# Kernel tuning notes

Hardware: AMD Instinct MI355X
Metric: run time of the kernel (lower is better)

## Reference

```python
import jax, jax.numpy as jnp
import numpy as np

START = 5.0
STEP = 8
SIZE = 256
STOP = SIZE // 2 - 1.0  # self.stop = int(size/2) - 1.0
# Original loops over tf.linspace(s, stop, step) and truncates each value to int.
US = [int(v) for v in np.linspace(START, STOP, STEP)]


def _block_mask(w, h, u):
    # Boolean block of ones of size (2u+1)^2 centered at (w//2, h//2).
    # Original: dd[half_w-u:half_w+u+1, half_h-u:half_h+u+1] = 1, then keeps
    # only that region of the shifted spectrum (ideal low-pass filter).
    m = np.zeros((w, h), dtype=np.float32)
    m[w // 2 - u: w // 2 + u + 1, h // 2 - u: h // 2 + u + 1] = 1.0
    return jnp.asarray(m)


def setup_inputs() -> dict:
    key = jax.random.key(0)
    x = jax.random.normal(key, (64, SIZE, SIZE, 1), dtype=jnp.float32)
    return {"x": x}


def reference(x):
    n, w, h, c = x.shape  # c == 1
    im = x[..., 0].astype(jnp.complex64)  # [n, w, h]
    # FFT is identical across loop iterations in the original; hoist it.
    # fftshift/ifftshift over all axes in TF cancel on the batch axis, so
    # shifting only the spatial axes is mathematically identical.
    freq = jnp.fft.fftshift(jnp.fft.fft2(im), axes=(-2, -1))
    outs = [x]
    for u in US:  # small fixed loop over STEP cutoff radii
        mask = _block_mask(w, h, u)
        low = freq * mask.astype(jnp.complex64)  # keep low frequencies only
        out = jnp.real(jnp.fft.ifft2(jnp.fft.ifftshift(low, axes=(-2, -1))))
        outs.append(out.astype(x.dtype)[..., None])
    return jnp.concatenate(outs, axis=-1)  # [n, w, h, STEP+1]
```

## Files before the change

### kernel.cpp

```cpp
#include <hip/hip_runtime.h>

typedef __attribute__((ext_vector_type(4))) float          f32x4;
typedef __attribute__((ext_vector_type(2))) float          f32x2;
typedef __attribute__((ext_vector_type(4))) unsigned int   u32x4;
typedef __attribute__((ext_vector_type(4))) unsigned short u16x4;
typedef __attribute__((ext_vector_type(2))) unsigned short u16x2;

typedef const unsigned int __attribute__((address_space(1)))* gas_ptr;
typedef unsigned int __attribute__((address_space(3)))*       las_ptr;

#define PI_F 3.14159265358979f

__device__ __forceinline__ unsigned short f2bf(float f) {
    unsigned int x = __float_as_uint(f);
    unsigned int r = ((x >> 16) & 1u) + 0x7fffu;
    return (unsigned short)((x + r) >> 16);
}
__device__ __forceinline__ float bf2f(unsigned short v) {
    return __uint_as_float((unsigned int)v << 16);
}
__device__ __forceinline__ void mfma16(f32x4& c, u32x4 a, u32x4 b) {
    asm volatile("v_mfma_f32_16x16x32_bf16 %0, %1, %2, %0"
                 : "+v"(c) : "v"(a), "v"(b));
}
__device__ __forceinline__ void gload16(const void* g, void* l) {
    __builtin_amdgcn_global_load_lds((gas_ptr)g, (las_ptr)l, 16, 0, 0);
}

#define SWZ(r, cb) (((unsigned)(r) * 128u) + ((unsigned)(cb) ^ ((((unsigned)(r)) & 7u) << 4)))

__global__ void prep(const float* __restrict__ x, unsigned short* __restrict__ H,
                     unsigned short* __restrict__ Xb, float* __restrict__ out,
                     int write_c0) {
    int b = blockIdx.x;
    if (b < 2048) {
        const int US[8] = {5, 22, 39, 57, 74, 92, 109, 127};
        int idx = b * 256 + threadIdx.x;
        int u = idx >> 16;
        int i = (idx >> 8) & 255, js = idx & 255;
        int jl = js ^ ((i & 7) << 3);
        int d = (i - jl) & 255;
        int m = 2 * US[u] + 1;
        float h;
        if (d == 0) {
            h = (float)m * (1.0f / 256.0f);
        } else {
            int t = (m * d) & 511;
            float num = sinf((float)t * (PI_F / 256.0f));
            float den = sinf((float)d * (PI_F / 256.0f));
            h = num / (256.0f * den);
        }
        H[idx] = f2bf(h);
    } else {
        int idx = (b - 2048) * 256 + threadIdx.x;
        f32x4 v = ((const f32x4*)x)[idx];
        u16x4 o = { f2bf(v.x), f2bf(v.y), f2bf(v.z), f2bf(v.w) };
        int n = idx >> 14;
        int t = idx & 16383;
        int i = t >> 6;
        int jlin = (t & 63) * 4;
        int js = jlin ^ ((i & 7) << 3);
        *(u16x4*)(Xb + (size_t)n * 65536 + i * 256 + js) = o;
        if (write_c0) {
            size_t g = (size_t)idx * 4;
            out[(g + 0) * 9] = v.x;
            out[(g + 1) * 9] = v.y;
            out[(g + 2) * 9] = v.z;
            out[(g + 3) * 9] = v.w;
        }
    }
}

__global__ void __launch_bounds__(512) stage12(const unsigned short* __restrict__ Xb,
                                               const unsigned short* __restrict__ H,
                                               unsigned short* __restrict__ Zb,
                                               float* __restrict__ fOut,
                                               int mode, int u_fixed) {
    extern __shared__ char smem[];
    char* sStage = smem;
    char* sHalf  = smem + 32768;
    char* sT     = smem + 49152;

    int n, u, jh;
    if (u_fixed >= 0) {
        n = blockIdx.x >> 1; jh = blockIdx.x & 1; u = u_fixed;
    } else {
        int swz = (blockIdx.x & 7) * 128 + (blockIdx.x >> 3);
        n = swz >> 4; u = (swz >> 1) & 7; jh = swz & 1;
    }

    const char* Xn = (const char*)(Xb + (size_t)n * 65536);
    const char* Hu = (const char*)(H + (size_t)u * 65536);

    const int tid  = threadIdx.x;
    const int lane = tid & 63;
    const int w    = tid >> 6;
    const int lrow = lane & 15;
    const int lk   = lane >> 4;
    const int srow = lane >> 3, sch = lane & 7;

    f32x4 acc[4][4];
#pragma unroll
    for (int a = 0; a < 4; ++a)
#pragma unroll
        for (int b = 0; b < 4; ++b) acc[a][b] = (f32x4){0.f, 0.f, 0.f, 0.f};

    const int wiA = w >> 1, wjA = w & 1;
    for (int kt = 0; kt < 4; ++kt) {
        if (kt) __syncthreads();
#pragma unroll
        for (int q = 0; q < 4; ++q) {
            int r = (w * 4 + q) * 8 + srow;
            gload16(Xn + r * 512 + kt * 128 + sch * 16, sStage + (w * 4 + q) * 1024);
        }
#pragma unroll
        for (int q = 0; q < 2; ++q) {
            int r = jh * 128 + (w * 2 + q) * 8 + srow;
            gload16(Hu + r * 512 + kt * 128 + sch * 16, sHalf + (w * 2 + q) * 1024);
        }
        __syncthreads();
#pragma unroll
        for (int kk = 0; kk < 2; ++kk) {
            const int kb = kk * 64 + lk * 16;
            u32x4 af[4], bf[4];
#pragma unroll
            for (int mi = 0; mi < 4; ++mi)
                af[mi] = *(const u32x4*)(sStage + SWZ(wiA * 64 + mi * 16 + lrow, kb));
#pragma unroll
            for (int ni = 0; ni < 4; ++ni)
                bf[ni] = *(const u32x4*)(sHalf + SWZ(wjA * 64 + ni * 16 + lrow, kb));
#pragma unroll
            for (int mi = 0; mi < 4; ++mi)
#pragma unroll
                for (int ni = 0; ni < 4; ++ni)
                    mfma16(acc[mi][ni], af[mi], bf[ni]);
        }
    }
    asm volatile("s_nop 7\n\ts_nop 7");
#pragma unroll
    for (int mi = 0; mi < 4; ++mi) {
        int i4 = wiA * 64 + mi * 16 + (lane >> 4) * 4;
#pragma unroll
        for (int ni = 0; ni < 4; ++ni) {
            int jl = wjA * 64 + ni * 16 + lrow;
            u16x4 o = { f2bf(acc[mi][ni].x), f2bf(acc[mi][ni].y),
                        f2bf(acc[mi][ni].z), f2bf(acc[mi][ni].w) };
            *(u16x4*)(sT + jl * 512 + ((2 * i4) ^ ((jl & 7) << 4))) = o;
        }
    }
    __syncthreads();

#pragma unroll
    for (int a = 0; a < 4; ++a)
#pragma unroll
        for (int b = 0; b < 4; ++b) acc[a][b] = (f32x4){0.f, 0.f, 0.f, 0.f};

    const int wrB = w & 1, wcB = w >> 1;
    for (int kt = 0; kt < 4; ++kt) {
        if (kt) __syncthreads();
#pragma unroll
        for (int q = 0; q < 4; ++q) {
            int r = (w * 4 + q) * 8 + srow;
            gload16(Hu + r * 512 + kt * 128 + sch * 16, sStage + (w * 4 + q) * 1024);
        }
        __syncthreads();
#pragma unroll
        for (int kk = 0; kk < 2; ++kk) {
            const int kb  = kk * 64 + lk * 16;
            const int kbT = kt * 128 + kb;
            u32x4 af[4], bf[4];
#pragma unroll
            for (int mi = 0; mi < 4; ++mi) {
                int r = wrB * 64 + mi * 16 + lrow;
                af[mi] = *(const u32x4*)(sT + r * 512 + (kbT ^ ((r & 7) << 4)));
            }
#pragma unroll
            for (int ni = 0; ni < 4; ++ni)
                bf[ni] = *(const u32x4*)(sStage + SWZ(wcB * 64 + ni * 16 + lrow, kb));
#pragma unroll
            for (int mi = 0; mi < 4; ++mi)
#pragma unroll
                for (int ni = 0; ni < 4; ++ni)
                    mfma16(acc[mi][ni], af[mi], bf[ni]);
        }
    }
    asm volatile("s_nop 7\n\ts_nop 7");

    if (mode == 0) {
        unsigned short* Op = Zb + ((size_t)(u * 64 + n)) * 65536 + jh * 128;
#pragma unroll
        for (int mi = 0; mi < 4; ++mi) {
            int r4 = wrB * 64 + mi * 16 + (lane >> 4) * 4;
#pragma unroll
            for (int ni = 0; ni < 4; ++ni) {
                int c = wcB * 64 + ni * 16 + lrow;
                u16x4 o = { f2bf(acc[mi][ni].x), f2bf(acc[mi][ni].y),
                            f2bf(acc[mi][ni].z), f2bf(acc[mi][ni].w) };
                *(u16x4*)(Op + (size_t)c * 256 + r4) = o;
            }
        }
    } else {
#pragma unroll
        for (int mi = 0; mi < 4; ++mi) {
            int r4 = wrB * 64 + mi * 16 + (lane >> 4) * 4;
#pragma unroll
            for (int ni = 0; ni < 4; ++ni) {
                int c = wcB * 64 + ni * 16 + lrow;
                float* o = fOut + (((size_t)n * 256 + c) * 256 + jh * 128 + r4) * 9 + 1 + u;
                o[0]  = acc[mi][ni].x;
                o[9]  = acc[mi][ni].y;
                o[18] = acc[mi][ni].z;
                o[27] = acc[mi][ni].w;
            }
        }
    }
}

__global__ void __launch_bounds__(256) pack9(const float* __restrict__ x,
                                             const unsigned short* __restrict__ Zb,
                                             float* __restrict__ out) {
    __shared__ float sl[9216];
    const int t = threadIdx.x;
    const size_t g0 = (size_t)blockIdx.x * 1024;

#pragma unroll
    for (int c = 0; c < 2; ++c) {
        int q = c * 512 + t * 2;
        size_t p = g0 + q;
        f32x2 xv = *(const f32x2*)(x + p);
        sl[q * 9]       = xv.x;
        sl[(q + 1) * 9] = xv.y;
#pragma unroll
        for (int u = 0; u < 8; ++u) {
            u16x2 z = *(const u16x2*)(Zb + (size_t)u * 4194304 + p);
            sl[q * 9 + 1 + u]       = bf2f(z.x);
            sl[(q + 1) * 9 + 1 + u] = bf2f(z.y);
        }
    }
    __syncthreads();
    float* ob = out + g0 * 9;
#pragma unroll
    for (int r = 0; r < 9; ++r) {
        int d = r * 1024 + t * 4;
        *(f32x4*)(ob + d) = *(const f32x4*)&sl[d];
    }
}

extern "C" void kernel_launch(void* const* d_in, const int* in_sizes, int n_in,
                              void* d_out, int out_size, void* d_ws, size_t ws_size,
                              hipStream_t stream) {
    const float* x = (const float*)d_in[0];
    float* out = (float*)d_out;
    char* ws = (char*)d_ws;

    unsigned short* H  = (unsigned short*)(ws);
    unsigned short* Xb = (unsigned short*)(ws + 1048576);
    unsigned short* Zb = (unsigned short*)(ws + 9437184);

    const size_t NEED_FULL = 76546048ull;
    const size_t LDS_BYTES = 114688;

    if (ws_size >= NEED_FULL) {
        prep<<<6144, 256, 0, stream>>>(x, H, Xb, out, 0);
        stage12<<<1024, 512, LDS_BYTES, stream>>>(Xb, H, Zb, nullptr, 0, -1);
        pack9<<<4096, 256, 0, stream>>>(x, Zb, out);
    } else {
        prep<<<6144, 256, 0, stream>>>(x, H, Xb, out, 1);
        for (int u = 0; u < 8; ++u)
            stage12<<<128, 512, LDS_BYTES, stream>>>(Xb, H, nullptr, out, 1, u);
    }
}
```

Before: 102.1 us.

## Split stage12 into quarter-column blocks with 4 waves and smaller LDS

Each stage12 block now computes a 64-column quarter instead of a half, running 256 threads (4 waves) and using less LDS. The grid doubles to 2048 blocks with a new swizzled mapping. The goal is higher occupancy and more blocks per CU from the smaller LDS footprint. In exchange, the full 256-row X tile and the H matrix in the second GEMM are reloaded twice as often, so redundant global and LDS traffic rises.

```diff
diff --git a/kernel.cpp b/kernel.cpp
--- a/kernel.cpp
+++ b/kernel.cpp
@@ -71,22 +71,22 @@
     }
 }
 
-__global__ void __launch_bounds__(512) stage12(const unsigned short* __restrict__ Xb,
+__global__ void __launch_bounds__(256) stage12(const unsigned short* __restrict__ Xb,
                                                const unsigned short* __restrict__ H,
                                                unsigned short* __restrict__ Zb,
                                                float* __restrict__ fOut,
                                                int mode, int u_fixed) {
     extern __shared__ char smem[];
     char* sStage = smem;
-    char* sHalf  = smem + 32768;
-    char* sT     = smem + 49152;
-
-    int n, u, jh;
+    char* sHq    = smem + 32768;
+    char* sT     = smem + 40960;
+
+    int n, u, jq;
     if (u_fixed >= 0) {
-        n = blockIdx.x >> 1; jh = blockIdx.x & 1; u = u_fixed;
-    } else {
-        int swz = (blockIdx.x & 7) * 128 + (blockIdx.x >> 3);
-        n = swz >> 4; u = (swz >> 1) & 7; jh = swz & 1;
+        n = blockIdx.x >> 2; jq = blockIdx.x & 3; u = u_fixed;
+    } else {
+        int swz = (blockIdx.x & 7) * 256 + (blockIdx.x >> 3);
+        n = swz >> 5; u = (swz >> 2) & 7; jq = swz & 3;
     }
 
     const char* Xn = (const char*)(Xb + (size_t)n * 65536);
@@ -105,18 +105,17 @@
 #pragma unroll
         for (int b = 0; b < 4; ++b) acc[a][b] = (f32x4){0.f, 0.f, 0.f, 0.f};
 
-    const int wiA = w >> 1, wjA = w & 1;
     for (int kt = 0; kt < 4; ++kt) {
         if (kt) __syncthreads();
 #pragma unroll
-        for (int q = 0; q < 4; ++q) {
-            int r = (w * 4 + q) * 8 + srow;
-            gload16(Xn + r * 512 + kt * 128 + sch * 16, sStage + (w * 4 + q) * 1024);
+        for (int q = 0; q < 8; ++q) {
+            int r = (w * 8 + q) * 8 + srow;
+            gload16(Xn + r * 512 + kt * 128 + sch * 16, sStage + (w * 8 + q) * 1024);
         }
 #pragma unroll
         for (int q = 0; q < 2; ++q) {
-            int r = jh * 128 + (w * 2 + q) * 8 + srow;
-            gload16(Hu + r * 512 + kt * 128 + sch * 16, sHalf + (w * 2 + q) * 1024);
+            int r = jq * 64 + (w * 2 + q) * 8 + srow;
+            gload16(Hu + r * 512 + kt * 128 + sch * 16, sHq + (w * 2 + q) * 1024);
         }
         __syncthreads();
 #pragma unroll
@@ -125,10 +124,10 @@
             u32x4 af[4], bf[4];
 #pragma unroll
             for (int mi = 0; mi < 4; ++mi)
-                af[mi] = *(const u32x4*)(sStage + SWZ(wiA * 64 + mi * 16 + lrow, kb));
+                af[mi] = *(const u32x4*)(sStage + SWZ(w * 64 + mi * 16 + lrow, kb));
 #pragma unroll
             for (int ni = 0; ni < 4; ++ni)
-                bf[ni] = *(const u32x4*)(sHalf + SWZ(wjA * 64 + ni * 16 + lrow, kb));
+                bf[ni] = *(const u32x4*)(sHq + SWZ(ni * 16 + lrow, kb));
 #pragma unroll
             for (int mi = 0; mi < 4; ++mi)
 #pragma unroll
@@ -137,12 +136,13 @@
         }
     }
     asm volatile("s_nop 7\n\ts_nop 7");
+
 #pragma unroll
     for (int mi = 0; mi < 4; ++mi) {
-        int i4 = wiA * 64 + mi * 16 + (lane >> 4) * 4;
+        int i4 = w * 64 + mi * 16 + (lane >> 4) * 4;
 #pragma unroll
         for (int ni = 0; ni < 4; ++ni) {
-            int jl = wjA * 64 + ni * 16 + lrow;
+            int jl = ni * 16 + lrow;
             u16x4 o = { f2bf(acc[mi][ni].x), f2bf(acc[mi][ni].y),
                         f2bf(acc[mi][ni].z), f2bf(acc[mi][ni].w) };
             *(u16x4*)(sT + jl * 512 + ((2 * i4) ^ ((jl & 7) << 4))) = o;
@@ -155,13 +155,12 @@
 #pragma unroll
         for (int b = 0; b < 4; ++b) acc[a][b] = (f32x4){0.f, 0.f, 0.f, 0.f};
 
-    const int wrB = w & 1, wcB = w >> 1;
     for (int kt = 0; kt < 4; ++kt) {
         if (kt) __syncthreads();
 #pragma unroll
-        for (int q = 0; q < 4; ++q) {
-            int r = (w * 4 + q) * 8 + srow;
-            gload16(Hu + r * 512 + kt * 128 + sch * 16, sStage + (w * 4 + q) * 1024);
+        for (int q = 0; q < 8; ++q) {
+            int r = (w * 8 + q) * 8 + srow;
+            gload16(Hu + r * 512 + kt * 128 + sch * 16, sStage + (w * 8 + q) * 1024);
         }
         __syncthreads();
 #pragma unroll
@@ -171,12 +170,12 @@
             u32x4 af[4], bf[4];
 #pragma unroll
             for (int mi = 0; mi < 4; ++mi) {
-                int r = wrB * 64 + mi * 16 + lrow;
+                int r = mi * 16 + lrow;
                 af[mi] = *(const u32x4*)(sT + r * 512 + (kbT ^ ((r & 7) << 4)));
             }
 #pragma unroll
             for (int ni = 0; ni < 4; ++ni)
-                bf[ni] = *(const u32x4*)(sStage + SWZ(wcB * 64 + ni * 16 + lrow, kb));
+                bf[ni] = *(const u32x4*)(sStage + SWZ(w * 64 + ni * 16 + lrow, kb));
 #pragma unroll
             for (int mi = 0; mi < 4; ++mi)
 #pragma unroll
@@ -187,13 +186,13 @@
     asm volatile("s_nop 7\n\ts_nop 7");
 
     if (mode == 0) {
-        unsigned short* Op = Zb + ((size_t)(u * 64 + n)) * 65536 + jh * 128;
+        unsigned short* Op = Zb + ((size_t)(u * 64 + n)) * 65536 + jq * 64;
 #pragma unroll
         for (int mi = 0; mi < 4; ++mi) {
-            int r4 = wrB * 64 + mi * 16 + (lane >> 4) * 4;
+            int r4 = mi * 16 + (lane >> 4) * 4;
 #pragma unroll
             for (int ni = 0; ni < 4; ++ni) {
-                int c = wcB * 64 + ni * 16 + lrow;
+                int c = w * 64 + ni * 16 + lrow;
                 u16x4 o = { f2bf(acc[mi][ni].x), f2bf(acc[mi][ni].y),
                             f2bf(acc[mi][ni].z), f2bf(acc[mi][ni].w) };
                 *(u16x4*)(Op + (size_t)c * 256 + r4) = o;
@@ -202,11 +201,11 @@
     } else {
 #pragma unroll
         for (int mi = 0; mi < 4; ++mi) {
-            int r4 = wrB * 64 + mi * 16 + (lane >> 4) * 4;
+            int r4 = mi * 16 + (lane >> 4) * 4;
 #pragma unroll
             for (int ni = 0; ni < 4; ++ni) {
-                int c = wcB * 64 + ni * 16 + lrow;
-                float* o = fOut + (((size_t)n * 256 + c) * 256 + jh * 128 + r4) * 9 + 1 + u;
+                int c = w * 64 + ni * 16 + lrow;
+                float* o = fOut + (((size_t)n * 256 + c) * 256 + jq * 64 + r4) * 9 + 1 + u;
                 o[0]  = acc[mi][ni].x;
                 o[9]  = acc[mi][ni].y;
                 o[18] = acc[mi][ni].z;
@@ -258,15 +257,15 @@
     unsigned short* Zb = (unsigned short*)(ws + 9437184);
 
     const size_t NEED_FULL = 76546048ull;
-    const size_t LDS_BYTES = 114688;
+    const size_t LDS_BYTES = 73728;
 
     if (ws_size >= NEED_FULL) {
         prep<<<6144, 256, 0, stream>>>(x, H, Xb, out, 0);
-        stage12<<<1024, 512, LDS_BYTES, stream>>>(Xb, H, Zb, nullptr, 0, -1);
+        stage12<<<2048, 256, LDS_BYTES, stream>>>(Xb, H, Zb, nullptr, 0, -1);
         pack9<<<4096, 256, 0, stream>>>(x, Zb, out);
     } else {
         prep<<<6144, 256, 0, stream>>>(x, H, Xb, out, 1);
         for (int u = 0; u < 8; ++u)
-            stage12<<<128, 512, LDS_BYTES, stream>>>(Xb, H, nullptr, out, 1, u);
-    }
-}
+            stage12<<<256, 256, LDS_BYTES, stream>>>(Xb, H, nullptr, out, 1, u);
+    }
+}
```

New measurement: 96.54 us. -5.5%, faster.
